# Kernel optimization log

Measured on AMD Instinct MI355X. Metric: run time of the kernel, lower is better.

## Reference

```python
import jax, jax.numpy as jnp
import numpy as np

B, S, H, R, K, L = 8, 2048, 512, 7, 10, 4
OFFSETS = np.array([-3, -2, -1, 1, 2, 3], dtype=np.int32)
BN_EPS = 1e-5


def setup_inputs() -> dict:
    key = jax.random.key(0)
    ks = jax.random.split(key, 12)
    u = lambda k, shape, s: jax.random.uniform(k, shape, minval=-s, maxval=s, dtype=jnp.float32)
    s3, sh, shr = 1.0 / np.sqrt(3.0), 1.0 / np.sqrt(H), 1.0 / np.sqrt(R * H)
    return {
        "n_coords": jax.random.normal(ks[0], (B, S, 3), jnp.float32),
        "ca_coords": jax.random.normal(ks[1], (B, S, 3), jnp.float32),
        "c_coords": jax.random.normal(ks[2], (B, S, 3), jnp.float32),
        "Wp": u(ks[3], (H, 3), s3),
        "bp": u(ks[4], (H,), s3),
        "Wlin": u(ks[5], (L, H, R * H), shr),
        "blin": u(ks[6], (L, H), shr),
        "Wself": u(ks[7], (L, H, H), sh),
        "bself": u(ks[8], (L, H), sh),
        "bn_gamma": jnp.ones((L, H), jnp.float32),
        "bn_beta": jnp.zeros((L, H), jnp.float32),
        "bn_mean": jax.random.normal(ks[9], (L, H), jnp.float32) * 0.1,
        "bn_var": jax.random.uniform(ks[10], (L, H), minval=0.5, maxval=1.5, dtype=jnp.float32),
    }


def _edges(pos):
    """Edge list per graph: sequential offsets -3..3 -> relations 0..5, KNN(k=10) -> relation 6."""
    i = jnp.arange(S)
    off = jnp.asarray(OFFSETS)
    dst_seq = i[:, None] + off[None, :]                            # [S,6]
    valid = (dst_seq >= 0) & (dst_seq < S)
    src_seq = jnp.broadcast_to(i[:, None], (S, 6))
    rel_seq = jnp.broadcast_to(jnp.arange(6, dtype=jnp.int32)[None, :], (S, 6))
    dst_seq = jnp.clip(dst_seq, 0, S - 1)
    # squared distances give the same topk-smallest ordering as torch.norm
    d2 = jnp.sum((pos[:, None, :] - pos[None, :, :]) ** 2, axis=-1)  # [S,S]
    _, knn = jax.lax.top_k(-d2, K + 1)                             # k+1 smallest, self first
    dst_knn = knn[:, 1:]                                           # drop self
    src_knn = jnp.broadcast_to(i[:, None], (S, K))
    rel_knn = jnp.full((S, K), 6, dtype=jnp.int32)
    src = jnp.concatenate([src_seq.reshape(-1), src_knn.reshape(-1)])
    dst = jnp.concatenate([dst_seq.reshape(-1), dst_knn.reshape(-1)])
    rel = jnp.concatenate([rel_seq.reshape(-1), rel_knn.reshape(-1)])
    w = jnp.concatenate([valid.reshape(-1).astype(pos.dtype),
                         jnp.ones((S * K,), pos.dtype)])
    return src, dst, rel, w


def _gearnet(ca_coords, Wp, bp, Wlin, blin, Wself, bself, bn_gamma, bn_beta, bn_mean, bn_var):
    def per_graph(pos):
        src, dst, rel, w = _edges(pos)
        seg = dst * R + rel                                        # node_out*num_relation + relation
        h = pos @ Wp.T + bp                                        # coord_projection: Linear(3, H)
        for l in range(L):
            msg = h[src] * w[:, None]                              # [E,H] gather + edge weight
            upd = jax.ops.segment_sum(msg, seg, num_segments=S * R)  # scatter-add per (node, relation)
            upd = upd.reshape(S, R * H)
            out = upd @ Wlin[l].T + blin[l] + h @ Wself[l].T + bself[l]
            out = (out - bn_mean[l]) * jax.lax.rsqrt(bn_var[l] + BN_EPS) * bn_gamma[l] + bn_beta[l]
            h = jax.nn.relu(out) + h                               # relu then short_cut residual
        return h
    return jax.vmap(per_graph)(ca_coords)                          # [B,S,H]


def reference(n_coords, ca_coords, c_coords, Wp, bp, Wlin, blin, Wself, bself,
              bn_gamma, bn_beta, bn_mean, bn_var):
    # n_coords / c_coords are accepted but unused, exactly as in the original forward.
    return _gearnet(ca_coords, Wp, bp, Wlin, blin, Wself, bself,
                    bn_gamma, bn_beta, bn_mean, bn_var)
```

## Files before the change

kernel.cpp:

```cpp
#include <hip/hip_runtime.h>
#include <stdint.h>

#define B_ 8
#define S_ 2048
#define H_ 512
#define R_ 7
#define K_ 10
#define L_ 4
#define KT_ 4096
#define RH_ 3584

typedef __attribute__((ext_vector_type(8))) short bf16x8;
typedef __attribute__((ext_vector_type(4))) float f32x4;
typedef __attribute__((ext_vector_type(4))) unsigned short u16x4;
typedef unsigned long long u64;

__device__ __forceinline__ unsigned short f2bf(float f){
  unsigned int u = __float_as_uint(f);
  u = (u + 0x7fffu + ((u >> 16) & 1u)) >> 16;
  return (unsigned short)u;
}

__device__ __forceinline__ float bf2f(unsigned short s){
  return __uint_as_float(((unsigned int)s) << 16);
}

__device__ __forceinline__ f32x4 bf4load(const unsigned short* p){
  u16x4 v = *(const u16x4*)p;
  f32x4 o;
#pragma unroll
  for (int e = 0; e < 4; e++) o[e] = bf2f(v[e]);
  return o;
}

__device__ __forceinline__ void gload16(const void* g, void* lds){
  __builtin_amdgcn_global_load_lds(
      (const __attribute__((address_space(1))) unsigned int*)g,
      (__attribute__((address_space(3))) unsigned int*)lds, 16, 0, 0);
}

__global__ __launch_bounds__(256) void knn_kernel(const float* __restrict__ pos,
                                                  int* __restrict__ knn){
  __shared__ float4 p4[S_];
  int b = blockIdx.y;
  const float* p = pos + (size_t)b * S_ * 3;
  for (int idx = threadIdx.x; idx < S_; idx += 256){
    float4 v; v.x = p[idx*3+0]; v.y = p[idx*3+1]; v.z = p[idx*3+2]; v.w = 0.f;
    p4[idx] = v;
  }
  __syncthreads();
  int w = threadIdx.x >> 6, l = threadIdx.x & 63;
#pragma unroll 1
  for (int q = 0; q < 4; ++q){
    int i = blockIdx.x * 16 + w * 4 + q;
    float4 pi = p4[i];
    float xi = pi.x, yi = pi.y, zi = pi.z;
    u64 best[10];
#pragma unroll
    for (int t = 0; t < 10; t++) best[t] = ~0ull;
    for (int j = l; j < S_; j += 64){
      if (j == i) continue;
      float4 pj = p4[j];
      float dx = __fsub_rn(xi, pj.x);
      float dy = __fsub_rn(yi, pj.y);
      float dz = __fsub_rn(zi, pj.z);
      float d2 = __fadd_rn(__fadd_rn(__fmul_rn(dx,dx), __fmul_rn(dy,dy)), __fmul_rn(dz,dz));
      u64 key = ((u64)__float_as_uint(d2) << 32) | (unsigned)j;
      if (key < best[9]){
        best[9] = key;
#pragma unroll
        for (int t = 9; t > 0; --t){
          u64 a = best[t-1], c = best[t];
          u64 lo = a < c ? a : c, hi = a < c ? c : a;
          best[t-1] = lo; best[t] = hi;
        }
      }
    }
    int* out = knn + ((size_t)b * S_ + i) * K_;
#pragma unroll
    for (int t = 0; t < 10; t++){
      u64 cand = best[0];
      u64 m = cand;
#pragma unroll
      for (int o = 32; o; o >>= 1){
        u64 other = __shfl_xor(m, o);
        if (other < m) m = other;
      }
      if (cand == m){
#pragma unroll
        for (int qq = 0; qq < 9; qq++) best[qq] = best[qq+1];
        best[9] = ~0ull;
      }
      if (l == 0) out[t] = (int)(unsigned)(m & 0xffffffffu);
    }
  }
}

__global__ void count_kernel(const int* __restrict__ knn, int* __restrict__ counts){
  int idx = blockIdx.x * 256 + threadIdx.x;
  int b = idx / (S_ * K_);
  int d = knn[idx];
  atomicAdd(&counts[b * S_ + d], 1);
}

__global__ __launch_bounds__(256) void scan_kernel(const int* __restrict__ counts,
                                                   int* __restrict__ row_start,
                                                   int* __restrict__ cursor){
  __shared__ int lds[256];
  int b = blockIdx.x, t = threadIdx.x;
  int base = b * S_;
  int v[8]; int s = 0;
#pragma unroll
  for (int e = 0; e < 8; e++){ v[e] = s; s += counts[base + t*8 + e]; }
  lds[t] = s;
  __syncthreads();
  int total = s;
  for (int o = 1; o < 256; o <<= 1){
    int add = 0;
    if (t >= o) add = lds[t - o];
    __syncthreads();
    lds[t] += add;
    __syncthreads();
  }
  int ex = lds[t] - total;
  int rb = b * (S_ + 1);
#pragma unroll
  for (int e = 0; e < 8; e++){
    int val = ex + v[e];
    row_start[rb + t*8 + e] = val;
    cursor[base + t*8 + e] = val;
  }
  if (t == 255) row_start[rb + S_] = lds[255];
}

__global__ void fill_kernel(const int* __restrict__ knn, int* __restrict__ cursor,
                            int* __restrict__ col){
  int idx = blockIdx.x * 256 + threadIdx.x;
  int b = idx / (S_ * K_);
  int i = (idx / K_) % S_;
  int d = knn[idx];
  int p = atomicAdd(&cursor[b * S_ + d], 1);
  col[(size_t)b * S_ * K_ + p] = i;
}

__global__ void sort_kernel(const int* __restrict__ row_start, int* __restrict__ col){
  int idx = blockIdx.x * 256 + threadIdx.x;
  int b = idx / S_, d = idx % S_;
  int rs = row_start[b*(S_+1)+d], re = row_start[b*(S_+1)+d+1];
  int* c = col + (size_t)b * S_ * K_;
  for (int a = rs + 1; a < re; ++a){
    int vv = c[a]; int q = a - 1;
    while (q >= rs && c[q] > vv){ c[q+1] = c[q]; --q; }
    c[q+1] = vv;
  }
}

__global__ void prepw_kernel(const float* __restrict__ Wlin, const float* __restrict__ Wself,
                             unsigned short* __restrict__ Wt){
  size_t e = ((size_t)blockIdx.x * 256 + threadIdx.x) * 8;
  int k = (int)(e & 4095);
  int j = (int)((e >> 12) & 511);
  int l = (int)(e >> 21);
  const float* src = (k < RH_) ? Wlin + ((size_t)l * H_ + j) * RH_ + k
                               : Wself + ((size_t)l * H_ + j) * H_ + (k - RH_);
  union { unsigned short s[8]; uint4 u; } pk;
#pragma unroll
  for (int t = 0; t < 8; t++) pk.s[t] = f2bf(src[t]);
  *(uint4*)&Wt[e] = pk.u;
}

__global__ void prepa_kernel(const float* __restrict__ gam, const float* __restrict__ bet,
                             const float* __restrict__ mean, const float* __restrict__ var,
                             const float* __restrict__ blin, const float* __restrict__ bself,
                             float* __restrict__ scale, float* __restrict__ shift){
  int idx = blockIdx.x * 256 + threadIdx.x;
  float sc = gam[idx] * rsqrtf(var[idx] + 1e-5f);
  scale[idx] = sc;
  shift[idx] = bet[idx] + (blin[idx] + bself[idx] - mean[idx]) * sc;
}

__global__ void inith_kernel(const float* __restrict__ pos, const float* __restrict__ Wp,
                             const float* __restrict__ bp, float* __restrict__ h,
                             unsigned short* __restrict__ hb){
  int idx = blockIdx.x * 256 + threadIdx.x;
  int j = (idx & 127) * 4;
  int bs = idx >> 7;
  const float* p = pos + (size_t)bs * 3;
  float x = p[0], y = p[1], z = p[2];
  f32x4 o;
#pragma unroll
  for (int e = 0; e < 4; e++){
    const float* wr = Wp + (j + e) * 3;
    o[e] = x * wr[0] + y * wr[1] + z * wr[2] + bp[j + e];
  }
  *(f32x4*)&h[(size_t)bs * H_ + j] = o;
  unsigned int w0 = f2bf(o[0]) | ((unsigned)f2bf(o[1]) << 16);
  unsigned int w1 = f2bf(o[2]) | ((unsigned)f2bf(o[3]) << 16);
  uint2 u; u.x = w0; u.y = w1;
  *(uint2*)&hb[(size_t)bs * H_ + j] = u;
}

__global__ __launch_bounds__(128) void hknn_kernel(const unsigned short* __restrict__ hb,
                                                   const int* __restrict__ row_start,
                                                   const int* __restrict__ col,
                                                   unsigned short* __restrict__ hk){
  int bx = blockIdx.x;
  int d = (bx & 7) * 256 + (bx >> 3);
  int b = blockIdx.y;
  int j = threadIdx.x * 4;
  int rs = row_start[b * (S_ + 1) + d];
  int re = row_start[b * (S_ + 1) + d + 1];
  const int* cl = col + (size_t)b * S_ * K_;
  f32x4 acc = {0.f, 0.f, 0.f, 0.f};
  for (int e = rs; e < re; ++e){
    int i = cl[e];
    acc += bf4load(&hb[((size_t)b * S_ + i) * H_ + j]);
  }
  u16x4 v;
#pragma unroll
  for (int e = 0; e < 4; e++) v[e] = f2bf(acc[e]);
  *(u16x4*)&hk[((size_t)b * S_ + d) * H_ + j] = v;
}

__global__ __launch_bounds__(512) void gemmf_kernel(
    const unsigned short* __restrict__ hbin,
    const unsigned short* __restrict__ hkn,
    const unsigned short* __restrict__ Wt,
    float* __restrict__ h,
    unsigned short* __restrict__ hbout,
    const float* __restrict__ scale,
    const float* __restrict__ shift,
    const unsigned short* __restrict__ zbuf){
  __shared__ unsigned short As[3][128 * 64];
  __shared__ unsigned short Bs[3][256 * 64];
  int tid = threadIdx.x;
  int wg = blockIdx.x;
  int swz = (wg & 7) * 32 + (wg >> 3);
  int my = swz >> 1;
  int nx = swz & 1;
  int l = tid & 63, wid = tid >> 6;
  int wm = wid >> 2, wn = wid & 3;
  f32x4 acc[4][4] = {};

  int arow = tid >> 3;
  int lA8 = ((tid & 7) ^ (arow & 7)) << 3;
  int gr0 = my * 128 + arow, gr1 = gr0 + 64;
  const unsigned short* Bp0 = Wt + (size_t)(nx * 256 +   0 + arow) * KT_ + lA8;
  const unsigned short* Bp1 = Wt + (size_t)(nx * 256 +  64 + arow) * KT_ + lA8;
  const unsigned short* Bp2 = Wt + (size_t)(nx * 256 + 128 + arow) * KT_ + lA8;
  const unsigned short* Bp3 = Wt + (size_t)(nx * 256 + 192 + arow) * KT_ + lA8;
  const unsigned short *sa0, *sa1;

#define SETSLC(rr) do {                                                       \
    int _r = (rr);                                                            \
    const unsigned short *_b0, *_b1;                                          \
    if (_r < 6){                                                              \
      int _sh = (_r < 3) ? (3 - _r) : (2 - _r);          \
      int _s0 = gr0 + _sh, _s1 = gr1 + _sh;                                   \
      _b0 = (((unsigned)_s0 >> 11) == ((unsigned)gr0 >> 11)) ? hbin + (size_t)_s0 * H_ : zbuf; \
      _b1 = (((unsigned)_s1 >> 11) == ((unsigned)gr1 >> 11)) ? hbin + (size_t)_s1 * H_ : zbuf; \
    } else {                                                                  \
      const unsigned short* _bb = (_r == 6) ? hkn : hbin;                     \
      _b0 = _bb + (size_t)gr0 * H_; _b1 = _bb + (size_t)gr1 * H_;             \
    }                                                                         \
    sa0 = _b0 + lA8; sa1 = _b1 + lA8;                                         \
  } while (0)

  int dA0 = tid * 8, dA1 = (512 + tid) * 8;
  int dB0 = tid * 8, dB1 = (512 + tid) * 8, dB2 = (1024 + tid) * 8, dB3 = (1536 + tid) * 8;

#define STAGE(sl, ko, kb) do {                             \
    gload16(sa0 + (ko), &As[sl][dA0]);                     \
    gload16(sa1 + (ko), &As[sl][dA1]);                     \
    gload16(Bp0 + (kb), &Bs[sl][dB0]);                     \
    gload16(Bp1 + (kb), &Bs[sl][dB1]);                     \
    gload16(Bp2 + (kb), &Bs[sl][dB2]);                     \
    gload16(Bp3 + (kb), &Bs[sl][dB3]);                     \
  } while (0)

  SETSLC(0);
  STAGE(0, 0, 0);
  STAGE(1, 64, 64);

  int kcr = l >> 4, lr = l & 15, lr7 = l & 7;
  int rA0 = wm * 64 + lr, rB0 = wn * 64 + lr;
  int pc0 = (kcr ^ lr7) * 8;
  int pc1 = ((4 + kcr) ^ lr7) * 8;
  int s = 0;
#pragma unroll 1
  for (int t = 0; t < 64; ++t){
    int s2 = s + 2; if (s2 >= 3) s2 -= 3;
    int tt = t + 2;
    bool st = (t < 62);
    if (st) SETSLC(tt >> 3);

    if (t < 63) asm volatile("s_waitcnt vmcnt(6)" ::: "memory");
    else        asm volatile("s_waitcnt vmcnt(0)" ::: "memory");
    __builtin_amdgcn_s_barrier();
    asm volatile("" ::: "memory");

    bf16x8 af0[4], af1[4], bf0[4], bf1[4];
#pragma unroll
    for (int mi = 0; mi < 4; mi++)
      af0[mi] = *(const bf16x8*)&As[s][(rA0 + mi * 16) * 64 + pc0];
#pragma unroll
    for (int ni = 0; ni < 4; ni++)
      bf0[ni] = *(const bf16x8*)&Bs[s][(rB0 + ni * 16) * 64 + pc0];
    __builtin_amdgcn_sched_barrier(0);
#pragma unroll
    for (int mi = 0; mi < 4; mi++)
      af1[mi] = *(const bf16x8*)&As[s][(rA0 + mi * 16) * 64 + pc1];
#pragma unroll
    for (int ni = 0; ni < 4; ni++)
      bf1[ni] = *(const bf16x8*)&Bs[s][(rB0 + ni * 16) * 64 + pc1];
    __builtin_amdgcn_sched_barrier(0);

    asm volatile("s_waitcnt lgkmcnt(8)" ::: "memory");
    __builtin_amdgcn_sched_barrier(0);
    __builtin_amdgcn_s_setprio(1);
#pragma unroll
    for (int mi = 0; mi < 4; mi++)
#pragma unroll
      for (int ni = 0; ni < 4; ni++)
        acc[mi][ni] = __builtin_amdgcn_mfma_f32_16x16x32_bf16(af0[mi], bf0[ni], acc[mi][ni], 0, 0, 0);
    __builtin_amdgcn_s_setprio(0);
    __builtin_amdgcn_sched_barrier(0);

    if (st) STAGE(s2, (tt & 7) * 64, tt * 64);

    asm volatile("s_waitcnt lgkmcnt(0)" ::: "memory");
    __builtin_amdgcn_sched_barrier(0);
    __builtin_amdgcn_s_setprio(1);
#pragma unroll
    for (int mi = 0; mi < 4; mi++)
#pragma unroll
      for (int ni = 0; ni < 4; ni++)
        acc[mi][ni] = __builtin_amdgcn_mfma_f32_16x16x32_bf16(af1[mi], bf1[ni], acc[mi][ni], 0, 0, 0);
    __builtin_amdgcn_s_setprio(0);
    asm volatile("" ::: "memory");
    __builtin_amdgcn_s_barrier();
    asm volatile("" ::: "memory");
    ++s; if (s == 3) s = 0;
  }
#undef STAGE
#undef SETSLC

  int r0 = (l >> 4) * 4, c0 = l & 15;
#pragma unroll
  for (int ni = 0; ni < 4; ni++){
    int gcol = nx * 256 + wn * 64 + ni * 16 + c0;
    float sc = scale[gcol], sf = shift[gcol];
#pragma unroll
    for (int mi = 0; mi < 4; mi++){
#pragma unroll
      for (int reg = 0; reg < 4; reg++){
        int grow = my * 128 + wm * 64 + mi * 16 + r0 + reg;
        size_t o = (size_t)grow * H_ + gcol;
        float val = fmaxf(acc[mi][ni][reg] * sc + sf, 0.f);
        float hv = h[o] + val;
        h[o] = hv;
        hbout[o] = f2bf(hv);
      }
    }
  }
}

extern "C" void kernel_launch(void* const* d_in, const int* in_sizes, int n_in,
                              void* d_out, int out_size, void* d_ws, size_t ws_size,
                              hipStream_t stream){
  const float* ca    = (const float*)d_in[1];
  const float* Wp    = (const float*)d_in[3];
  const float* bp    = (const float*)d_in[4];
  const float* Wlin  = (const float*)d_in[5];
  const float* blin  = (const float*)d_in[6];
  const float* Wself = (const float*)d_in[7];
  const float* bself = (const float*)d_in[8];
  const float* gam   = (const float*)d_in[9];
  const float* bet   = (const float*)d_in[10];
  const float* mean  = (const float*)d_in[11];
  const float* var   = (const float*)d_in[12];
  float* h = (float*)d_out;

  char* ws = (char*)d_ws;
  size_t off = 0;
  auto alloc = [&](size_t bytes) -> char* {
    char* p = ws + off;
    off = (off + bytes + 255) & ~(size_t)255;
    return p;
  };
  int* knn       = (int*)alloc((size_t)B_ * S_ * K_ * 4);
  int* counts    = (int*)alloc((size_t)B_ * S_ * 4);
  int* row_start = (int*)alloc((size_t)B_ * (S_ + 1) * 4);
  int* cursor    = (int*)alloc((size_t)B_ * S_ * 4);
  int* col       = (int*)alloc((size_t)B_ * S_ * K_ * 4);
  unsigned short* Wt  = (unsigned short*)alloc((size_t)L_ * H_ * KT_ * 2);
  float* scale   = (float*)alloc((size_t)L_ * H_ * 4);
  float* shift   = (float*)alloc((size_t)L_ * H_ * 4);
  unsigned short* hbA = (unsigned short*)alloc((size_t)B_ * S_ * H_ * 2);
  unsigned short* hbB = (unsigned short*)alloc((size_t)B_ * S_ * H_ * 2);
  unsigned short* hkn = (unsigned short*)alloc((size_t)B_ * S_ * H_ * 2);
  unsigned short* zbuf = (unsigned short*)alloc(4096 * 2);

  hipMemsetAsync(counts, 0, (size_t)B_ * S_ * 4, stream);
  hipMemsetAsync(zbuf, 0, 4096 * 2, stream);
  knn_kernel<<<dim3(S_ / 16, B_), 256, 0, stream>>>(ca, knn);
  count_kernel<<<dim3(B_ * S_ * K_ / 256), 256, 0, stream>>>(knn, counts);
  scan_kernel<<<dim3(B_), 256, 0, stream>>>(counts, row_start, cursor);
  fill_kernel<<<dim3(B_ * S_ * K_ / 256), 256, 0, stream>>>(knn, cursor, col);
  sort_kernel<<<dim3(B_ * S_ / 256), 256, 0, stream>>>(row_start, col);
  prepw_kernel<<<dim3((int)((size_t)L_ * H_ * KT_ / 8 / 256)), 256, 0, stream>>>(Wlin, Wself, Wt);
  prepa_kernel<<<dim3(L_ * H_ / 256), 256, 0, stream>>>(gam, bet, mean, var, blin, bself, scale, shift);
  inith_kernel<<<dim3(B_ * S_ * (H_ / 4) / 256), 256, 0, stream>>>(ca, Wp, bp, h, hbA);

  for (int l = 0; l < L_; l++){
    unsigned short* in  = (l & 1) ? hbB : hbA;
    unsigned short* out = (l & 1) ? hbA : hbB;
    hknn_kernel<<<dim3(S_, B_), 128, 0, stream>>>(in, row_start, col, hkn);
    gemmf_kernel<<<dim3(256), 512, 0, stream>>>(
        in, hkn, Wt + (size_t)l * H_ * KT_, h, out,
        scale + l * H_, shift + l * H_, zbuf);
  }
}
```

Measured before the change: 567.3 us.

## Spread KNN queries across more blocks, widen gather loads, merge GEMM barriers

```diff
diff --git a/kernel.cpp b/kernel.cpp
--- a/kernel.cpp
+++ b/kernel.cpp
@@ -50,49 +50,49 @@
   }
   __syncthreads();
   int w = threadIdx.x >> 6, l = threadIdx.x & 63;
+  int i = blockIdx.x * 4 + w;
+  float4 pi = p4[i];
+  float xi = pi.x, yi = pi.y, zi = pi.z;
+  u64 best[10];
+#pragma unroll
+  for (int q = 0; q < 10; q++) best[q] = ~0ull;
+  float4 nxt = p4[l];
 #pragma unroll 1
-  for (int q = 0; q < 4; ++q){
-    int i = blockIdx.x * 16 + w * 4 + q;
-    float4 pi = p4[i];
-    float xi = pi.x, yi = pi.y, zi = pi.z;
-    u64 best[10];
-#pragma unroll
-    for (int t = 0; t < 10; t++) best[t] = ~0ull;
-    for (int j = l; j < S_; j += 64){
-      if (j == i) continue;
-      float4 pj = p4[j];
-      float dx = __fsub_rn(xi, pj.x);
-      float dy = __fsub_rn(yi, pj.y);
-      float dz = __fsub_rn(zi, pj.z);
-      float d2 = __fadd_rn(__fadd_rn(__fmul_rn(dx,dx), __fmul_rn(dy,dy)), __fmul_rn(dz,dz));
-      u64 key = ((u64)__float_as_uint(d2) << 32) | (unsigned)j;
-      if (key < best[9]){
-        best[9] = key;
-#pragma unroll
-        for (int t = 9; t > 0; --t){
-          u64 a = best[t-1], c = best[t];
-          u64 lo = a < c ? a : c, hi = a < c ? c : a;
-          best[t-1] = lo; best[t] = hi;
-        }
+  for (int j = l; j < S_; j += 64){
+    float4 cur = nxt;
+    if (j + 64 < S_) nxt = p4[j + 64];
+    float dx = __fsub_rn(xi, cur.x);
+    float dy = __fsub_rn(yi, cur.y);
+    float dz = __fsub_rn(zi, cur.z);
+    float d2 = __fadd_rn(__fadd_rn(__fmul_rn(dx,dx), __fmul_rn(dy,dy)), __fmul_rn(dz,dz));
+    u64 key = ((u64)__float_as_uint(d2) << 32) | (unsigned)j;
+    key = (j == i) ? ~0ull : key;
+    if (key < best[9]){
+      best[9] = key;
+#pragma unroll
+      for (int q = 9; q > 0; --q){
+        u64 a = best[q-1], c = best[q];
+        u64 lo = a < c ? a : c, hi = a < c ? c : a;
+        best[q-1] = lo; best[q] = hi;
       }
     }
-    int* out = knn + ((size_t)b * S_ + i) * K_;
-#pragma unroll
-    for (int t = 0; t < 10; t++){
-      u64 cand = best[0];
-      u64 m = cand;
-#pragma unroll
-      for (int o = 32; o; o >>= 1){
-        u64 other = __shfl_xor(m, o);
-        if (other < m) m = other;
-      }
-      if (cand == m){
-#pragma unroll
-        for (int qq = 0; qq < 9; qq++) best[qq] = best[qq+1];
-        best[9] = ~0ull;
-      }
-      if (l == 0) out[t] = (int)(unsigned)(m & 0xffffffffu);
+  }
+  int* out = knn + ((size_t)b * S_ + i) * K_;
+#pragma unroll
+  for (int t = 0; t < 10; t++){
+    u64 cand = best[0];
+    u64 m = cand;
+#pragma unroll
+    for (int o = 32; o; o >>= 1){
+      u64 other = __shfl_xor(m, o);
+      if (other < m) m = other;
     }
+    if (cand == m){
+#pragma unroll
+      for (int q = 0; q < 9; q++) best[q] = best[q+1];
+      best[9] = ~0ull;
+    }
+    if (l == 0) out[t] = (int)(unsigned)(m & 0xffffffffu);
   }
 }
 
@@ -200,26 +200,45 @@
   *(uint2*)&hb[(size_t)bs * H_ + j] = u;
 }
 
-__global__ __launch_bounds__(128) void hknn_kernel(const unsigned short* __restrict__ hb,
+__global__ __launch_bounds__(256) void hknn_kernel(const unsigned short* __restrict__ hb,
                                                    const int* __restrict__ row_start,
                                                    const int* __restrict__ col,
                                                    unsigned short* __restrict__ hk){
-  int bx = blockIdx.x;
-  int d = (bx & 7) * 256 + (bx >> 3);
+  int w = threadIdx.x >> 6, l = threadIdx.x & 63;
+  int d = blockIdx.x * 4 + w;
   int b = blockIdx.y;
-  int j = threadIdx.x * 4;
   int rs = row_start[b * (S_ + 1) + d];
   int re = row_start[b * (S_ + 1) + d + 1];
   const int* cl = col + (size_t)b * S_ * K_;
-  f32x4 acc = {0.f, 0.f, 0.f, 0.f};
-  for (int e = rs; e < re; ++e){
-    int i = cl[e];
-    acc += bf4load(&hb[((size_t)b * S_ + i) * H_ + j]);
-  }
-  u16x4 v;
-#pragma unroll
-  for (int e = 0; e < 4; e++) v[e] = f2bf(acc[e]);
-  *(u16x4*)&hk[((size_t)b * S_ + d) * H_ + j] = v;
+  const unsigned short* base = hb + (size_t)b * S_ * H_ + l * 8;
+  f32x4 aLo = {0,0,0,0}, aHi = {0,0,0,0}, bLo = {0,0,0,0}, bHi = {0,0,0,0};
+  int e = rs;
+  for (; e + 1 < re; e += 2){
+    uint4 v0 = *(const uint4*)(base + (size_t)cl[e]     * H_);
+    uint4 v1 = *(const uint4*)(base + (size_t)cl[e + 1] * H_);
+    aLo[0] += __uint_as_float(v0.x << 16); aLo[1] += __uint_as_float(v0.x & 0xffff0000u);
+    aLo[2] += __uint_as_float(v0.y << 16); aLo[3] += __uint_as_float(v0.y & 0xffff0000u);
+    aHi[0] += __uint_as_float(v0.z << 16); aHi[1] += __uint_as_float(v0.z & 0xffff0000u);
+    aHi[2] += __uint_as_float(v0.w << 16); aHi[3] += __uint_as_float(v0.w & 0xffff0000u);
+    bLo[0] += __uint_as_float(v1.x << 16); bLo[1] += __uint_as_float(v1.x & 0xffff0000u);
+    bLo[2] += __uint_as_float(v1.y << 16); bLo[3] += __uint_as_float(v1.y & 0xffff0000u);
+    bHi[0] += __uint_as_float(v1.z << 16); bHi[1] += __uint_as_float(v1.z & 0xffff0000u);
+    bHi[2] += __uint_as_float(v1.w << 16); bHi[3] += __uint_as_float(v1.w & 0xffff0000u);
+  }
+  if (e < re){
+    uint4 v0 = *(const uint4*)(base + (size_t)cl[e] * H_);
+    aLo[0] += __uint_as_float(v0.x << 16); aLo[1] += __uint_as_float(v0.x & 0xffff0000u);
+    aLo[2] += __uint_as_float(v0.y << 16); aLo[3] += __uint_as_float(v0.y & 0xffff0000u);
+    aHi[0] += __uint_as_float(v0.z << 16); aHi[1] += __uint_as_float(v0.z & 0xffff0000u);
+    aHi[2] += __uint_as_float(v0.w << 16); aHi[3] += __uint_as_float(v0.w & 0xffff0000u);
+  }
+  aLo += bLo; aHi += bHi;
+  uint4 o;
+  o.x = f2bf(aLo[0]) | ((unsigned)f2bf(aLo[1]) << 16);
+  o.y = f2bf(aLo[2]) | ((unsigned)f2bf(aLo[3]) << 16);
+  o.z = f2bf(aHi[0]) | ((unsigned)f2bf(aHi[1]) << 16);
+  o.w = f2bf(aHi[2]) | ((unsigned)f2bf(aHi[3]) << 16);
+  *(uint4*)(hk + ((size_t)b * S_ + d) * H_ + l * 8) = o;
 }
 
 __global__ __launch_bounds__(512) void gemmf_kernel(
@@ -281,6 +300,9 @@
   SETSLC(0);
   STAGE(0, 0, 0);
   STAGE(1, 64, 64);
+  asm volatile("s_waitcnt vmcnt(6)" ::: "memory");
+  __builtin_amdgcn_s_barrier();
+  asm volatile("" ::: "memory");
 
   int kcr = l >> 4, lr = l & 15, lr7 = l & 7;
   int rA0 = wm * 64 + lr, rB0 = wn * 64 + lr;
@@ -294,11 +316,6 @@
     bool st = (t < 62);
     if (st) SETSLC(tt >> 3);
 
-    if (t < 63) asm volatile("s_waitcnt vmcnt(6)" ::: "memory");
-    else        asm volatile("s_waitcnt vmcnt(0)" ::: "memory");
-    __builtin_amdgcn_s_barrier();
-    asm volatile("" ::: "memory");
-
     bf16x8 af0[4], af1[4], bf0[4], bf1[4];
 #pragma unroll
     for (int mi = 0; mi < 4; mi++)
@@ -338,8 +355,13 @@
         acc[mi][ni] = __builtin_amdgcn_mfma_f32_16x16x32_bf16(af1[mi], bf1[ni], acc[mi][ni], 0, 0, 0);
     __builtin_amdgcn_s_setprio(0);
     asm volatile("" ::: "memory");
-    __builtin_amdgcn_s_barrier();
-    asm volatile("" ::: "memory");
+
+    if (t < 62)       asm volatile("s_waitcnt vmcnt(6)" ::: "memory");
+    else if (t == 62) asm volatile("s_waitcnt vmcnt(0)" ::: "memory");
+    if (t < 63){
+      __builtin_amdgcn_s_barrier();
+      asm volatile("" ::: "memory");
+    }
     ++s; if (s == 3) s = 0;
   }
 #undef STAGE
@@ -403,7 +425,7 @@
 
   hipMemsetAsync(counts, 0, (size_t)B_ * S_ * 4, stream);
   hipMemsetAsync(zbuf, 0, 4096 * 2, stream);
-  knn_kernel<<<dim3(S_ / 16, B_), 256, 0, stream>>>(ca, knn);
+  knn_kernel<<<dim3(S_ / 4, B_), 256, 0, stream>>>(ca, knn);
   count_kernel<<<dim3(B_ * S_ * K_ / 256), 256, 0, stream>>>(knn, counts);
   scan_kernel<<<dim3(B_), 256, 0, stream>>>(counts, row_start, cursor);
   fill_kernel<<<dim3(B_ * S_ * K_ / 256), 256, 0, stream>>>(knn, cursor, col);
@@ -415,7 +437,7 @@
   for (int l = 0; l < L_; l++){
     unsigned short* in  = (l & 1) ? hbB : hbA;
     unsigned short* out = (l & 1) ? hbA : hbB;
-    hknn_kernel<<<dim3(S_, B_), 128, 0, stream>>>(in, row_start, col, hkn);
+    hknn_kernel<<<dim3(S_ / 4, B_), 256, 0, stream>>>(in, row_start, col, hkn);
     gemmf_kernel<<<dim3(256), 512, 0, stream>>>(
         in, hkn, Wt + (size_t)l * H_ * KT_, h, out,
         scale + l * H_, shift + l * H_, zbuf);
```

Result: no change. 564.2 us (-0.5%).
